# Kernel tuning notes

Hardware: AMD Instinct MI355X
Metric: run time of the kernel (lower is better)

## Reference

```python
import jax, jax.numpy as jnp
import numpy as np
import math

B, S, E, H, D = 2, 2048, 1024, 16, 64  # batch, seq, embed, heads, head_dim


def setup_inputs() -> dict:
    key = jax.random.key(0)
    ks = jax.random.split(key, 10)
    scale = 1.0 / math.sqrt(D)
    return {
        "query": jax.random.normal(ks[0], (B, S, E), jnp.float32),
        "key": jax.random.normal(ks[1], (B, S, E), jnp.float32),
        "value": jax.random.normal(ks[2], (B, S, E), jnp.float32),
        "mask": jax.random.randint(ks[3], (1, 1, S, S), 0, 2, jnp.int32),
        # nn.Linear(single_dim, single_dim) weights (out,in) and biases
        "Wq": jax.random.uniform(ks[4], (D, D), jnp.float32, -scale, scale),
        "bq": jax.random.uniform(ks[5], (D,), jnp.float32, -scale, scale),
        "Wk": jax.random.uniform(ks[6], (D, D), jnp.float32, -scale, scale),
        "bk": jax.random.uniform(ks[7], (D,), jnp.float32, -scale, scale),
        "Wv": jax.random.uniform(ks[8], (D, D), jnp.float32, -scale, scale),
        "bv": jax.random.uniform(ks[9], (D,), jnp.float32, -scale, scale),
    }


def reference(query, key, value, mask, Wq, bq, Wk, bk, Wv, bv):
    b, sq, _ = query.shape
    sk = key.shape[1]
    # (b, s, E) -> (b, H, s, D)
    q = query.reshape(b, sq, H, D).transpose(0, 2, 1, 3)
    k = key.reshape(b, sk, H, D).transpose(0, 2, 1, 3)
    v = value.reshape(b, sk, H, D).transpose(0, 2, 1, 3)
    # per-head shared Linear on last dim: x @ W^T + b
    q = jnp.einsum('bhsd,ed->bhse', q, Wq) + bq
    k = jnp.einsum('bhsd,ed->bhse', k, Wk) + bk
    v = jnp.einsum('bhsd,ed->bhse', v, Wv) + bv
    scores = jnp.einsum('bhqd,bhkd->bhqk', q, k) / math.sqrt(D)
    scores = jnp.where(mask == 0, jnp.float32(-1e20), scores)
    attn = jax.nn.softmax(scores, axis=-1)
    out = jnp.einsum('bhqk,bhkd->bhqd', attn, v)
    return out.transpose(0, 2, 1, 3).reshape(b, sq, H * D)
```

## Files before the change

kernel.cpp:

```cpp
#include <hip/hip_runtime.h>

#define S_LEN 2048
#define E_DIM 1024
#define NH 16
#define HD 64
#define NT (S_LEN / 64)
#define SCALE_L2E 0.18033688011112042f
#define DEFER_THR 8.0f

typedef __bf16 bf16;
typedef __attribute__((ext_vector_type(4))) bf16 bf16x4;
typedef __attribute__((ext_vector_type(8))) bf16 bf16x8;
typedef __attribute__((ext_vector_type(4))) float f32x4;
typedef unsigned long long u64;
typedef unsigned int u32;

#define MFMA(a, b, c) __builtin_amdgcn_mfma_f32_16x16x32_bf16((a), (b), (c), 0, 0, 0)

__device__ __forceinline__ bf16x8 cvt8(f32x4 a, f32x4 b) {
  bf16x8 r;
  r[0] = (bf16)a[0]; r[1] = (bf16)a[1]; r[2] = (bf16)a[2]; r[3] = (bf16)a[3];
  r[4] = (bf16)b[0]; r[5] = (bf16)b[1]; r[6] = (bf16)b[2]; r[7] = (bf16)b[3];
  return r;
}

__device__ __forceinline__ bf16x8 load_cvt_frag(const float* p) {
  f32x4 a = *(const f32x4*)(p);
  f32x4 b = *(const f32x4*)(p + 16);
  return cvt8(a, b);
}

__global__ __launch_bounds__(256) void kvproj_k(
    const float* __restrict__ Kin, const float* __restrict__ Vin,
    const float* __restrict__ Wk, const float* __restrict__ bk,
    const float* __restrict__ Wv, const float* __restrict__ bv,
    const int* __restrict__ mask,
    bf16* __restrict__ KpF, bf16* __restrict__ VpF, u64* __restrict__ bits) {
  const int xcd = blockIdx.x & 7;
  const int idx = blockIdx.x >> 3;
  const int bh = xcd * 4 + (idx >> 5);
  const int sblk = idx & 31;
  const int h = bh & (NH - 1);
  const int b = bh >> 4;
  const int lane = threadIdx.x & 63;
  const int wave = threadIdx.x >> 6;
  const int g = lane >> 4;
  const int c16 = lane & 15;
  const int sbase = sblk * 64 + wave * 16;
  const int srow = sbase + c16;

  const float* xk = Kin + ((size_t)b * S_LEN + srow) * E_DIM + h * HD;
  const float* xv = Vin + ((size_t)b * S_LEN + srow) * E_DIM + h * HD;
  bf16x8 xkf[2], xvf[2];
#pragma unroll
  for (int c = 0; c < 2; ++c) {
    xkf[c] = load_cvt_frag(xk + 32 * c + 4 * g);
    xvf[c] = load_cvt_frag(xv + 32 * c + 4 * g);
  }

#pragma unroll
  for (int nt = 0; nt < 4; ++nt) {
    const float* wr = Wk + (16 * nt + c16) * HD + 4 * g;
    f32x4 acc = {0.f, 0.f, 0.f, 0.f};
    acc = MFMA(xkf[0], load_cvt_frag(wr), acc);
    acc = MFMA(xkf[1], load_cvt_frag(wr + 32), acc);
    const float bias = bk[16 * nt + c16];
    const size_t fidx = (((size_t)bh * 32 + sblk) * 4 + wave) * 2 + (nt >> 1);
    const int e = (c16 & 3) + 4 * (nt & 1);
#pragma unroll
    for (int r = 0; r < 4; ++r) {
      const int lane_p = (c16 >> 2) * 16 + 4 * g + r;
      KpF[fidx * 512 + lane_p * 8 + e] = (bf16)(acc[r] + bias);
    }
  }
#pragma unroll
  for (int nt = 0; nt < 4; ++nt) {
    const float* wr = Wv + (16 * nt + c16) * HD + 4 * g;
    f32x4 acc = {0.f, 0.f, 0.f, 0.f};
    acc = MFMA(load_cvt_frag(wr), xvf[0], acc);
    acc = MFMA(load_cvt_frag(wr + 32), xvf[1], acc);
    const size_t fidx = (((size_t)bh * 32 + sblk) * 4 + nt) * 2 + (wave >> 1);
    const int e = (c16 & 3) + 4 * (wave & 1);
#pragma unroll
    for (int r = 0; r < 4; ++r) {
      const int dout = 16 * nt + 4 * g + r;
      const int lane_p = (c16 >> 2) * 16 + 4 * g + r;
      VpF[fidx * 512 + lane_p * 8 + e] = (bf16)(acc[r] + bv[dout]);
    }
  }

  const int wbase = blockIdx.x * 64 + wave * 16;
  int mv[16];
#pragma unroll
  for (int i = 0; i < 16; ++i) mv[i] = mask[(size_t)(wbase + i) * 64 + lane];
#pragma unroll
  for (int i = 0; i < 16; ++i) {
    const u64 bb = __ballot(mv[i] != 0);
    const int w = wbase + i;
    if (lane == 0) bits[(size_t)(w & 31) * S_LEN + (w >> 5)] = bb;
  }
}

__global__ __launch_bounds__(256) void attn_k(
    const float* __restrict__ Qin, const float* __restrict__ Wq, const float* __restrict__ bq,
    const bf16* __restrict__ KpF, const bf16* __restrict__ VpF,
    const u64* __restrict__ mbits, float* __restrict__ out) {
  const int xcd = blockIdx.x & 7;
  const int idx = blockIdx.x >> 3;
  const int bh = xcd * 4 + (idx >> 4);
  const int qg4 = idx & 15;
  const int h = bh & (NH - 1);
  const int b = bh >> 4;
  const int lane = threadIdx.x & 63;
  const int wave = threadIdx.x >> 6;
  const int g = lane >> 4;
  const int c16 = lane & 15;
  const int qbase = (qg4 * 4 + wave) * 32;

  bf16x8 qfrag[2][2];
#pragma unroll
  for (int grp = 0; grp < 2; ++grp) {
    const int qrow = qbase + grp * 16 + c16;
    const float* xq = Qin + ((size_t)b * S_LEN + qrow) * E_DIM + h * HD;
    bf16x8 xqf[2];
#pragma unroll
    for (int c = 0; c < 2; ++c) xqf[c] = load_cvt_frag(xq + 32 * c + 4 * g);
    f32x4 qt[4];
#pragma unroll
    for (int t = 0; t < 4; ++t) {
      const float* wr = Wq + (16 * t + c16) * HD + 4 * g;
      f32x4 acc = {0.f, 0.f, 0.f, 0.f};
      acc = MFMA(load_cvt_frag(wr), xqf[0], acc);
      acc = MFMA(load_cvt_frag(wr + 32), xqf[1], acc);
#pragma unroll
      for (int r = 0; r < 4; ++r) acc[r] = (acc[r] + bq[16 * t + 4 * g + r]) * SCALE_L2E;
      qt[t] = acc;
    }
    qfrag[grp][0] = cvt8(qt[0], qt[1]);
    qfrag[grp][1] = cvt8(qt[2], qt[3]);
  }

  bf16x8 ones;
#pragma unroll
  for (int i = 0; i < 8; ++i) ones[i] = (bf16)1.0f;

  const bf16* ktl = KpF + ((size_t)bh * 32) * 4096 + lane * 8;
  const bf16* vtl = VpF + ((size_t)bh * 32) * 4096 + lane * 8;
  const u64* mrowA = mbits + (qbase + c16);
  const u64* mrowB = mrowA + 16;

  float m[2] = {-1e30f, -1e30f};
  f32x4 o[2][4] = {};
  f32x4 o5[2] = {};

  bf16x8 kfa[8], kfb[8], vfr[8];
  u64 mca[2], mcb[2];

#pragma unroll
  for (int f = 0; f < 8; ++f) kfa[f] = *(const bf16x8*)(ktl + f * 512);
  mca[0] = mrowA[0];
  mca[1] = mrowB[0];

#define PROCESS(CURK, NXTK, MWC, MWN, KBT)                                        \
  {                                                                               \
    const int nk = ((KBT) + 1 < NT) ? (KBT) + 1 : NT - 1;                         \
    _Pragma("unroll") for (int f = 0; f < 8; ++f)                                 \
        NXTK[f] = *(const bf16x8*)(ktl + (size_t)nk * 4096 + f * 512);            \
    MWN[0] = mrowA[(size_t)nk * S_LEN];                                           \
    MWN[1] = mrowB[(size_t)nk * S_LEN];                                           \
    _Pragma("unroll") for (int f = 0; f < 8; ++f)                                 \
        vfr[f] = *(const bf16x8*)(vtl + (size_t)(KBT) * 4096 + f * 512);          \
    _Pragma("unroll") for (int grp = 0; grp < 2; ++grp) {                         \
      f32x4 st[4];                                                                \
      __builtin_amdgcn_s_setprio(1);                                              \
      _Pragma("unroll") for (int ks = 0; ks < 4; ++ks) {                          \
        f32x4 acc = {0.f, 0.f, 0.f, 0.f};                                         \
        acc = MFMA(CURK[2 * ks], qfrag[grp][0], acc);                             \
        acc = MFMA(CURK[2 * ks + 1], qfrag[grp][1], acc);                         \
        st[ks] = acc;                                                             \
      }                                                                           \
      __builtin_amdgcn_s_setprio(0);                                              \
      const u64 mws = MWC[grp] >> (4 * g);                                        \
      const u32 mlo = (u32)mws;                                                   \
      const u32 mhi = (u32)(mws >> 32);                                           \
      const float t0 = fmaxf(fmaxf(st[0][0], st[0][1]), st[0][2]);                \
      const float t1 = fmaxf(fmaxf(st[0][3], st[1][0]), st[1][1]);                \
      const float t2 = fmaxf(fmaxf(st[1][2], st[1][3]), st[2][0]);                \
      const float t3 = fmaxf(fmaxf(st[2][1], st[2][2]), st[2][3]);                \
      const float t4 = fmaxf(fmaxf(st[3][0], st[3][1]), st[3][2]);                \
      const float tm =                                                            \
          fmaxf(fmaxf(fmaxf(t0, t1), t2), fmaxf(fmaxf(t3, t4), st[3][3]));        \
      if (!__all(tm <= m[grp] + DEFER_THR)) {                                     \
        float tmax = fmaxf(tm, __shfl_xor(tm, 16));                               \
        tmax = fmaxf(tmax, __shfl_xor(tmax, 32));                                 \
        const float mnew = fmaxf(m[grp], tmax);                                   \
        const float corr = __builtin_amdgcn_exp2f(m[grp] - mnew);                 \
        _Pragma("unroll") for (int t = 0; t < 4; ++t)                             \
            _Pragma("unroll") for (int r = 0; r < 4; ++r) o[grp][t][r] *= corr;   \
        _Pragma("unroll") for (int r = 0; r < 4; ++r) o5[grp][r] *= corr;         \
        m[grp] = mnew;                                                            \
      }                                                                           \
      _Pragma("unroll") for (int ks = 0; ks < 4; ++ks) {                          \
        const u32 mword = (ks < 2) ? mlo : mhi;                                   \
        const int base = (ks & 1) * 16;                                           \
        _Pragma("unroll") for (int r = 0; r < 4; ++r) {                           \
          const float p = __builtin_amdgcn_exp2f(st[ks][r] - m[grp]);             \
          const int keep = __builtin_amdgcn_sbfe(mword, base + r, 1);             \
          st[ks][r] = __uint_as_float(__float_as_uint(p) & (u32)keep);            \
        }                                                                         \
      }                                                                           \
      const bf16x8 pfrag0 = cvt8(st[0], st[1]);                                   \
      const bf16x8 pfrag1 = cvt8(st[2], st[3]);                                   \
      __builtin_amdgcn_s_setprio(1);                                              \
      _Pragma("unroll") for (int t = 0; t < 4; ++t) {                             \
        o[grp][t] = MFMA(vfr[2 * t], pfrag0, o[grp][t]);                          \
        o[grp][t] = MFMA(vfr[2 * t + 1], pfrag1, o[grp][t]);                      \
      }                                                                           \
      o5[grp] = MFMA(ones, pfrag0, o5[grp]);                                      \
      o5[grp] = MFMA(ones, pfrag1, o5[grp]);                                      \
      __builtin_amdgcn_s_setprio(0);                                              \
    }                                                                             \
  }

  for (int kb2 = 0; kb2 < NT; kb2 += 2) {
    PROCESS(kfa, kfb, mca, mcb, kb2);
    PROCESS(kfb, kfa, mcb, mca, kb2 + 1);
  }
#undef PROCESS

#pragma unroll
  for (int grp = 0; grp < 2; ++grp) {
    const float inv = 1.0f / o5[grp][0];
    float* orow = out + ((size_t)b * S_LEN + qbase + grp * 16 + c16) * E_DIM + h * HD;
#pragma unroll
    for (int t = 0; t < 4; ++t) {
      f32x4 v;
#pragma unroll
      for (int r = 0; r < 4; ++r) v[r] = o[grp][t][r] * inv;
      *(f32x4*)(orow + 16 * t + 4 * g) = v;
    }
  }
}

extern "C" void kernel_launch(void* const* d_in, const int* in_sizes, int n_in,
                              void* d_out, int out_size, void* d_ws, size_t ws_size,
                              hipStream_t stream) {
  const float* Q = (const float*)d_in[0];
  const float* K = (const float*)d_in[1];
  const float* V = (const float*)d_in[2];
  const int* mask = (const int*)d_in[3];
  const float* Wq = (const float*)d_in[4];
  const float* bq = (const float*)d_in[5];
  const float* Wk = (const float*)d_in[6];
  const float* bk = (const float*)d_in[7];
  const float* Wv = (const float*)d_in[8];
  const float* bv = (const float*)d_in[9];
  float* out = (float*)d_out;

  char* ws = (char*)d_ws;
  const size_t proj_bytes = (size_t)2 * NH * S_LEN * HD * 2;
  bf16* KpF = (bf16*)ws;
  bf16* VpF = (bf16*)(ws + proj_bytes);
  u64* mbits = (u64*)(ws + 2 * proj_bytes);

  kvproj_k<<<2 * NH * (S_LEN / 64), 256, 0, stream>>>(K, V, Wk, bk, Wv, bv, mask,
                                                      KpF, VpF, mbits);
  attn_k<<<2 * NH * (S_LEN / 128), 256, 0, stream>>>(Q, Wq, bq, KpF, VpF, mbits, out);
}
```

Before: 96.10 us.

## Split attention key range across wave pairs and merge partial softmax in LDS

Each block now covers 64 query rows instead of 128, and two waves share each 32-row query group, each processing half of the key tiles. The partial max, row sums and outputs go to shared memory and are merged with a rescaled (flash-decoding style) combine before the store. This doubles the grid to 1024 blocks to raise occupancy and parallelism, at the cost of redundant Q projection per split, extra LDS traffic and a block barrier. Launch bounds now request 4 blocks per CU, which may constrain registers.

```diff
diff --git a/kernel.cpp b/kernel.cpp
--- a/kernel.cpp
+++ b/kernel.cpp
@@ -5,6 +5,7 @@
 #define NH 16
 #define HD 64
 #define NT (S_LEN / 64)
+#define NTS (NT / 2)
 #define SCALE_L2E 0.18033688011112042f
 #define DEFER_THR 8.0f
 
@@ -101,21 +102,27 @@
   }
 }
 
-__global__ __launch_bounds__(256) void attn_k(
+__global__ __launch_bounds__(256, 4) void attn_k(
     const float* __restrict__ Qin, const float* __restrict__ Wq, const float* __restrict__ bq,
     const bf16* __restrict__ KpF, const bf16* __restrict__ VpF,
     const u64* __restrict__ mbits, float* __restrict__ out) {
   const int xcd = blockIdx.x & 7;
   const int idx = blockIdx.x >> 3;
-  const int bh = xcd * 4 + (idx >> 4);
-  const int qg4 = idx & 15;
+  const int bh = xcd * 4 + (idx >> 5);
+  const int qc = idx & 31;
   const int h = bh & (NH - 1);
   const int b = bh >> 4;
   const int lane = threadIdx.x & 63;
   const int wave = threadIdx.x >> 6;
   const int g = lane >> 4;
   const int c16 = lane & 15;
-  const int qbase = (qg4 * 4 + wave) * 32;
+  const int qg32 = wave >> 1;
+  const int split = wave & 1;
+  const int qbase = qc * 64 + qg32 * 32;
+
+  __shared__ float sm_m[2][2][2][16];
+  __shared__ float sm_l[2][2][2][16];
+  __shared__ float sm_o[2][2][2][16][65];
 
   bf16x8 qfrag[2][2];
 #pragma unroll
@@ -144,10 +151,9 @@
 #pragma unroll
   for (int i = 0; i < 8; ++i) ones[i] = (bf16)1.0f;
 
-  const bf16* ktl = KpF + ((size_t)bh * 32) * 4096 + lane * 8;
-  const bf16* vtl = VpF + ((size_t)bh * 32) * 4096 + lane * 8;
-  const u64* mrowA = mbits + (qbase + c16);
-  const u64* mrowB = mrowA + 16;
+  const bf16* ktl = KpF + ((size_t)bh * 32 + split * NTS) * 4096 + lane * 8;
+  const bf16* vtl = VpF + ((size_t)bh * 32 + split * NTS) * 4096 + lane * 8;
+  const u64* mrowT = mbits + (size_t)(split * NTS) * S_LEN + qbase + c16;
 
   float m[2] = {-1e30f, -1e30f};
   f32x4 o[2][4] = {};
@@ -158,18 +164,18 @@
 
 #pragma unroll
   for (int f = 0; f < 8; ++f) kfa[f] = *(const bf16x8*)(ktl + f * 512);
-  mca[0] = mrowA[0];
-  mca[1] = mrowB[0];
-
-#define PROCESS(CURK, NXTK, MWC, MWN, KBT)                                        \
+  mca[0] = mrowT[0];
+  mca[1] = mrowT[16];
+
+#define PROCESS(CURK, NXTK, MWC, MWN, IT)                                         \
   {                                                                               \
-    const int nk = ((KBT) + 1 < NT) ? (KBT) + 1 : NT - 1;                         \
+    const int nk = ((IT) + 1 < NTS) ? (IT) + 1 : NTS - 1;                         \
     _Pragma("unroll") for (int f = 0; f < 8; ++f)                                 \
         NXTK[f] = *(const bf16x8*)(ktl + (size_t)nk * 4096 + f * 512);            \
-    MWN[0] = mrowA[(size_t)nk * S_LEN];                                           \
-    MWN[1] = mrowB[(size_t)nk * S_LEN];                                           \
+    MWN[0] = mrowT[(size_t)nk * S_LEN];                                           \
+    MWN[1] = mrowT[(size_t)nk * S_LEN + 16];                                      \
     _Pragma("unroll") for (int f = 0; f < 8; ++f)                                 \
-        vfr[f] = *(const bf16x8*)(vtl + (size_t)(KBT) * 4096 + f * 512);          \
+        vfr[f] = *(const bf16x8*)(vtl + (size_t)(IT) * 4096 + f * 512);           \
     _Pragma("unroll") for (int grp = 0; grp < 2; ++grp) {                         \
       f32x4 st[4];                                                                \
       __builtin_amdgcn_s_setprio(1);                                              \
@@ -222,23 +228,49 @@
     }                                                                             \
   }
 
-  for (int kb2 = 0; kb2 < NT; kb2 += 2) {
-    PROCESS(kfa, kfb, mca, mcb, kb2);
-    PROCESS(kfb, kfa, mcb, mca, kb2 + 1);
+  for (int i2 = 0; i2 < NTS; i2 += 2) {
+    PROCESS(kfa, kfb, mca, mcb, i2);
+    PROCESS(kfb, kfa, mcb, mca, i2 + 1);
   }
 #undef PROCESS
 
-#pragma unroll
-  for (int grp = 0; grp < 2; ++grp) {
-    const float inv = 1.0f / o5[grp][0];
-    float* orow = out + ((size_t)b * S_LEN + qbase + grp * 16 + c16) * E_DIM + h * HD;
-#pragma unroll
-    for (int t = 0; t < 4; ++t) {
-      f32x4 v;
-#pragma unroll
-      for (int r = 0; r < 4; ++r) v[r] = o[grp][t][r] * inv;
-      *(f32x4*)(orow + 16 * t + 4 * g) = v;
-    }
+  if (g == 0) {
+#pragma unroll
+    for (int grp = 0; grp < 2; ++grp) {
+      sm_m[qg32][split][grp][c16] = m[grp];
+      sm_l[qg32][split][grp][c16] = o5[grp][0];
+    }
+  }
+#pragma unroll
+  for (int grp = 0; grp < 2; ++grp)
+#pragma unroll
+    for (int t = 0; t < 4; ++t)
+#pragma unroll
+      for (int r = 0; r < 4; ++r)
+        sm_o[qg32][split][grp][c16][16 * t + 4 * g + r] = o[grp][t][r];
+  __syncthreads();
+
+  const int og32 = wave >> 1;
+  const int og16 = wave & 1;
+  const float m0 = sm_m[og32][0][og16][c16];
+  const float m1 = sm_m[og32][1][og16][c16];
+  const float M = fmaxf(m0, m1);
+  const float cc0 = __builtin_amdgcn_exp2f(m0 - M);
+  const float cc1 = __builtin_amdgcn_exp2f(m1 - M);
+  const float lsum = cc0 * sm_l[og32][0][og16][c16] + cc1 * sm_l[og32][1][og16][c16];
+  const float w0 = cc0 / lsum;
+  const float w1 = cc1 / lsum;
+  const int orow_idx = qc * 64 + wave * 16 + c16;
+  float* orow = out + ((size_t)b * S_LEN + orow_idx) * E_DIM + h * HD;
+#pragma unroll
+  for (int t = 0; t < 4; ++t) {
+    f32x4 v;
+#pragma unroll
+    for (int r = 0; r < 4; ++r) {
+      const int col = 16 * t + 4 * g + r;
+      v[r] = w0 * sm_o[og32][0][og16][c16][col] + w1 * sm_o[og32][1][og16][c16][col];
+    }
+    *(f32x4*)(orow + 16 * t + 4 * g) = v;
   }
 }
 
@@ -265,5 +297,5 @@
 
   kvproj_k<<<2 * NH * (S_LEN / 64), 256, 0, stream>>>(K, V, Wk, bk, Wv, bv, mask,
                                                       KpF, VpF, mbits);
-  attn_k<<<2 * NH * (S_LEN / 128), 256, 0, stream>>>(Q, Wq, bq, KpF, VpF, mbits, out);
-}
+  attn_k<<<2 * NH * (S_LEN / 64), 256, 0, stream>>>(Q, Wq, bq, KpF, VpF, mbits, out);
+}
```

After: 284.4 us. +196.0%, slower.

## Stage K/V tiles cooperatively in triple-buffered LDS via global_load_lds

Applied to the files above, without the earlier changes.

Until now each of the four waves in a block loaded every K and V tile from global memory into its own registers, so each tile was fetched four times. Now the waves split each tile's load and copy it straight into a three-slot shared-memory buffer with global_load_lds, two tiles ahead. Each wave then reads its K and V fragments from LDS, with hand-placed vmcnt waits and a barrier after every tile. This cuts global/L2 traffic and register pressure. The cost is 48 KB of LDS per block, which may limit occupancy, plus per-tile barrier overhead.

```diff
diff --git a/kernel.cpp b/kernel.cpp
--- a/kernel.cpp
+++ b/kernel.cpp
@@ -108,14 +108,16 @@
   const int xcd = blockIdx.x & 7;
   const int idx = blockIdx.x >> 3;
   const int bh = xcd * 4 + (idx >> 4);
-  const int qg4 = idx & 15;
+  const int qc = idx & 15;
   const int h = bh & (NH - 1);
   const int b = bh >> 4;
   const int lane = threadIdx.x & 63;
   const int wave = threadIdx.x >> 6;
   const int g = lane >> 4;
   const int c16 = lane & 15;
-  const int qbase = (qg4 * 4 + wave) * 32;
+  const int qbase = qc * 128 + wave * 32;
+
+  __shared__ __align__(16) bf16 lds_kv[3][16 * 512];
 
   bf16x8 qfrag[2][2];
 #pragma unroll
@@ -144,45 +146,77 @@
 #pragma unroll
   for (int i = 0; i < 8; ++i) ones[i] = (bf16)1.0f;
 
-  const bf16* ktl = KpF + ((size_t)bh * 32) * 4096 + lane * 8;
-  const bf16* vtl = VpF + ((size_t)bh * 32) * 4096 + lane * 8;
-  const u64* mrowA = mbits + (qbase + c16);
-  const u64* mrowB = mrowA + 16;
+  const bf16* ktile = KpF + ((size_t)bh * 32) * 4096;
+  const bf16* vtile = VpF + ((size_t)bh * 32) * 4096;
+  const u64* mrowT = mbits + qbase + c16;
 
   float m[2] = {-1e30f, -1e30f};
   f32x4 o[2][4] = {};
   f32x4 o5[2] = {};
 
-  bf16x8 kfa[8], kfb[8], vfr[8];
+#define STAGE(BUF, T)                                                              \
+  {                                                                                \
+    const bf16* ks_ = ktile + (size_t)(T) * 4096 + (2 * wave) * 512 + lane * 8;    \
+    const bf16* vs_ = vtile + (size_t)(T) * 4096 + (2 * wave) * 512 + lane * 8;    \
+    __builtin_amdgcn_global_load_lds(                                              \
+        (const __attribute__((address_space(1))) u32*)ks_,                         \
+        (__attribute__((address_space(3))) u32*)((BUF) + (2 * wave) * 512), 16, 0, 0); \
+    __builtin_amdgcn_global_load_lds(                                              \
+        (const __attribute__((address_space(1))) u32*)(ks_ + 512),                 \
+        (__attribute__((address_space(3))) u32*)((BUF) + (2 * wave + 1) * 512), 16, 0, 0); \
+    __builtin_amdgcn_global_load_lds(                                              \
+        (const __attribute__((address_space(1))) u32*)vs_,                         \
+        (__attribute__((address_space(3))) u32*)((BUF) + 4096 + (2 * wave) * 512), 16, 0, 0); \
+    __builtin_amdgcn_global_load_lds(                                              \
+        (const __attribute__((address_space(1))) u32*)(vs_ + 512),                 \
+        (__attribute__((address_space(3))) u32*)((BUF) + 4096 + (2 * wave + 1) * 512), 16, 0, 0); \
+  }
+
+  bf16* b0 = &lds_kv[0][0];
+  bf16* b1 = &lds_kv[1][0];
+  bf16* b2 = &lds_kv[2][0];
+
   u64 mca[2], mcb[2];
 
-#pragma unroll
-  for (int f = 0; f < 8; ++f) kfa[f] = *(const bf16x8*)(ktl + f * 512);
-  mca[0] = mrowA[0];
-  mca[1] = mrowB[0];
-
-#define PROCESS(CURK, NXTK, MWC, MWN, KBT)                                        \
+  STAGE(b0, 0)
+  STAGE(b1, 1)
+  mca[0] = mrowT[0];
+  mca[1] = mrowT[16];
+  mcb[0] = mrowT[S_LEN];
+  mcb[1] = mrowT[S_LEN + 16];
+  asm volatile("s_waitcnt vmcnt(8)" ::: "memory");
+  asm volatile("s_barrier" ::: "memory");
+
+#define ITER(BUF, NXT, MREG, T)                                                   \
   {                                                                               \
-    const int nk = ((KBT) + 1 < NT) ? (KBT) + 1 : NT - 1;                         \
+    const u64 mw0_ = MREG[0];                                                     \
+    const u64 mw1_ = MREG[1];                                                     \
+    const bool more_ = (T) + 2 < NT;                                              \
+    if (more_) {                                                                  \
+      MREG[0] = mrowT[(size_t)((T) + 2) * S_LEN];                                 \
+      MREG[1] = mrowT[(size_t)((T) + 2) * S_LEN + 16];                            \
+      STAGE(NXT, (T) + 2)                                                         \
+    }                                                                             \
+    bf16x8 kf[8], vfr[8];                                                         \
     _Pragma("unroll") for (int f = 0; f < 8; ++f)                                 \
-        NXTK[f] = *(const bf16x8*)(ktl + (size_t)nk * 4096 + f * 512);            \
-    MWN[0] = mrowA[(size_t)nk * S_LEN];                                           \
-    MWN[1] = mrowB[(size_t)nk * S_LEN];                                           \
-    _Pragma("unroll") for (int f = 0; f < 8; ++f)                                 \
-        vfr[f] = *(const bf16x8*)(vtl + (size_t)(KBT) * 4096 + f * 512);          \
+        kf[f] = *(const bf16x8*)((BUF) + f * 512 + lane * 8);                     \
     _Pragma("unroll") for (int grp = 0; grp < 2; ++grp) {                         \
+      const u64 mws = ((grp == 0) ? mw0_ : mw1_) >> (4 * g);                      \
+      const u32 mlo = (u32)mws;                                                   \
+      const u32 mhi = (u32)(mws >> 32);                                           \
       f32x4 st[4];                                                                \
       __builtin_amdgcn_s_setprio(1);                                              \
       _Pragma("unroll") for (int ks = 0; ks < 4; ++ks) {                          \
         f32x4 acc = {0.f, 0.f, 0.f, 0.f};                                         \
-        acc = MFMA(CURK[2 * ks], qfrag[grp][0], acc);                             \
-        acc = MFMA(CURK[2 * ks + 1], qfrag[grp][1], acc);                         \
+        acc = MFMA(kf[2 * ks], qfrag[grp][0], acc);                               \
+        acc = MFMA(kf[2 * ks + 1], qfrag[grp][1], acc);                           \
         st[ks] = acc;                                                             \
       }                                                                           \
       __builtin_amdgcn_s_setprio(0);                                              \
-      const u64 mws = MWC[grp] >> (4 * g);                                        \
-      const u32 mlo = (u32)mws;                                                   \
-      const u32 mhi = (u32)(mws >> 32);                                           \
+      if (grp == 0) {                                                             \
+        _Pragma("unroll") for (int f = 0; f < 8; ++f)                             \
+            vfr[f] = *(const bf16x8*)((BUF) + 4096 + f * 512 + lane * 8);         \
+      }                                                                           \
       const float t0 = fmaxf(fmaxf(st[0][0], st[0][1]), st[0][2]);                \
       const float t1 = fmaxf(fmaxf(st[0][3], st[1][0]), st[1][1]);                \
       const float t2 = fmaxf(fmaxf(st[1][2], st[1][3]), st[2][0]);                \
@@ -220,13 +254,18 @@
       o5[grp] = MFMA(ones, pfrag1, o5[grp]);                                      \
       __builtin_amdgcn_s_setprio(0);                                              \
     }                                                                             \
-  }
-
-  for (int kb2 = 0; kb2 < NT; kb2 += 2) {
-    PROCESS(kfa, kfb, mca, mcb, kb2);
-    PROCESS(kfb, kfa, mcb, mca, kb2 + 1);
-  }
-#undef PROCESS
+    if (more_) asm volatile("s_waitcnt vmcnt(6)" ::: "memory");                   \
+    else       asm volatile("s_waitcnt vmcnt(0)" ::: "memory");                   \
+    asm volatile("s_barrier" ::: "memory");                                       \
+  }
+
+  for (int t = 0; t < NT; t += 2) {
+    ITER(b0, b2, mca, t)
+    ITER(b1, b0, mcb, t + 1)
+    bf16* tmp = b2; b2 = b1; b1 = b0; b0 = tmp;
+  }
+#undef ITER
+#undef STAGE
 
 #pragma unroll
   for (int grp = 0; grp < 2; ++grp) {
```

New measurement: 101.0 us. 1.05x slower.
